# Kernel optimization log

Measured on AMD Instinct MI355X. Metric: run time of the kernel, lower is better.

Reference implementation:

```python
import jax, jax.numpy as jnp
import numpy as np


def butterfly_mult(twiddle, x):
    # twiddle: (S, M, n//2, 2, 2); x: (B, S, n); increasing_stride=True
    B, S, n = x.shape
    M = twiddle.shape[1]
    out = x
    for idx in range(M):  # loop over log2(n) stages (structural, not data dim)
        stride = 1 << idx
        g = n // (2 * stride)
        t = twiddle[:, idx].reshape(S, g, stride, 2, 2)   # (S, g, r, i, j)
        xr = out.reshape(B, S, g, 2, stride)              # (B, S, g, j, r)
        out = jnp.einsum('sgrij,bsgjr->bsgir', t, xr).reshape(B, S, n)
    return out


def butterfly_layer(x, twiddle, bias, out_size):
    # x: (..., n) with n a power of 2 (pre_process pad is a no-op)
    lead = x.shape[:-1]
    n = x.shape[-1]
    S = twiddle.shape[0]
    xb = x.reshape(-1, n)
    xb = jnp.broadcast_to(xb[:, None, :], (xb.shape[0], S, n))  # expand to nstacks
    out = butterfly_mult(twiddle, xb)
    out = out.reshape(out.shape[0], S * n)[:, :out_size] + bias[:out_size]
    return out.reshape(*lead, out_size)


def setup_inputs() -> dict:
    key = jax.random.key(0)
    ks = jax.random.split(key, 5)
    B, T, D, H = 4, 4096, 1024, 4096
    inv_sqrt2 = 1.0 / np.sqrt(2.0).astype(np.float32)
    x = jax.random.normal(ks[0], (B, T, D), jnp.float32)
    tw1 = jax.random.normal(ks[1], (4, 10, 512, 2, 2), jnp.float32) * inv_sqrt2
    b1 = jax.random.normal(ks[2], (H,), jnp.float32) * 0.02
    tw2 = jax.random.normal(ks[3], (1, 11, 1024, 2, 2), jnp.float32) * inv_sqrt2
    b2 = jax.random.normal(ks[4], (D,), jnp.float32) * 0.02
    return {"x": x, "tw1": tw1, "b1": b1, "tw2": tw2, "b2": b2}


def reference(x, tw1, b1, tw2, b2):
    # GLU: fc1 (butterfly) -> chunk -> x * sigmoid(gates) -> fc2 (butterfly)
    h = butterfly_layer(x, tw1, b1, 4096)      # (B, T, 4096)
    a, gates = jnp.split(h, 2, axis=-1)        # (B, T, 2048) each
    h = a * jax.nn.sigmoid(gates)
    return butterfly_layer(h, tw2, b2, 1024)   # (B, T, 1024)
```

## Files before the change

kernel.cpp:

```cpp
#include <hip/hip_runtime.h>
#include <cstdint>


typedef float          v4f __attribute__((ext_vector_type(4)));
typedef unsigned int   u4i __attribute__((ext_vector_type(4)));
typedef unsigned int   u2i __attribute__((ext_vector_type(2)));
typedef short          bf8 __attribute__((ext_vector_type(8)));

#define MFMA16(A, B, C) __builtin_amdgcn_mfma_f32_16x16x32_bf16(A, B, C, 0, 0, 0)

__device__ __forceinline__ unsigned pk2(float a, float b) {
    unsigned ua = __float_as_uint(a) + 0x8000u;
    unsigned ub = __float_as_uint(b) + 0x8000u;
    return __builtin_amdgcn_perm(ub, ua, 0x07060302u);
}

__device__ __forceinline__ float sigmf(float g) {
    return __builtin_amdgcn_rcpf(1.0f + __expf(-g));
}
__device__ __forceinline__ v4f sig4(v4f g) {
    v4f r; r.x = sigmf(g.x); r.y = sigmf(g.y); r.z = sigmf(g.z); r.w = sigmf(g.w);
    return r;
}

__device__ __forceinline__ int ab(int row, int hw) {
    return (row << 11) + (((hw) << 1) ^ ((row & 7) << 4));
}

__global__ void build_mats(const float* __restrict__ tw1,
                           const float* __restrict__ tw2,
                           unsigned short* __restrict__ wsm)
{
    const int mid = blockIdx.x * 2 + (threadIdx.x >> 5);
    const int c   = threadIdx.x & 31;

    const float* twf; int np, rbase, rstep, j0, scaleb = -1, l2s = 0;
    if (mid < 128)      { twf = tw1 + (mid >> 5) * 20480;        np = 512;  rbase = (mid & 31) * 32; rstep = 1;  j0 = 0; }
    else if (mid < 256) { twf = tw1 + ((mid - 128) >> 5) * 20480; np = 512; rbase = mid & 31;        rstep = 32; j0 = 5; }
    else if (mid < 320) { twf = tw2; np = 1024; rbase = (mid - 256) * 32; rstep = 1; j0 = 0; }
    else                { twf = tw2; np = 1024; l2s = mid & 31; scaleb = (mid - 320) >> 5;
                          rbase = l2s + (scaleb << 10); rstep = 32; j0 = 5; }

    float v[32];
    #pragma unroll
    for (int r = 0; r < 32; ++r) v[r] = (r == c) ? 1.0f : 0.0f;

    #pragma unroll
    for (int jj = 0; jj < 5; ++jj) {
        const int j = j0 + jj;
        #pragma unroll
        for (int pr = 0; pr < 16; ++pr) {
            const int r0   = ((pr >> jj) << (jj + 1)) | (pr & ((1 << jj) - 1));
            const int r1   = r0 | (1 << jj);
            const int p0   = rbase + r0 * rstep;
            const int tidx = ((p0 >> (j + 1)) << j) | (p0 & ((1 << j) - 1));
            const v4f T    = *(const v4f*)(twf + (size_t)(j * np + tidx) * 4);
            const float a = v[r0], b = v[r1];
            v[r0] = T.x * a + T.y * b;
            v[r1] = T.z * a + T.w * b;
        }
    }
    if (scaleb >= 0) {
        #pragma unroll
        for (int r = 0; r < 32; ++r)
            v[r] *= tw2[(size_t)(10 * 1024 + l2s + 32 * r) * 4 + scaleb];
    }
    #pragma unroll
    for (int r = 0; r < 32; ++r) {
        const int mt   = r >> 4;
        const int lane = (r & 15) + ((c >> 3) << 4);
        wsm[((size_t)(mid * 2 + mt) * 64 + lane) * 8 + (c & 7)] =
            (unsigned short)((__float_as_uint(v[r]) + 0x8000u) >> 16);
    }
}

__global__ __launch_bounds__(512) void glu_bfly(
    const float* __restrict__ x, const float* __restrict__ b1,
    const float* __restrict__ b2, const bf8* __restrict__ mats,
    float* __restrict__ out)
{
    extern __shared__ char lds[];
    char*  actA = lds;
    char*  actB = lds + 65536;
    float* b1t  = (float*)(lds + 131072);

    const int t = threadIdx.x, w = t >> 6, l = t & 63, lr = l & 15, lk = l >> 4;
    const int row0 = blockIdx.x * 32;
    const v4f vz = {0.f, 0.f, 0.f, 0.f};

    {
        const v4f* bp = (const v4f*)(b1 + t * 8);
        const v4f a = bp[0], b = bp[1];
        const float vals[8] = {a.x, a.y, a.z, a.w, b.x, b.y, b.z, b.w};
        #pragma unroll
        for (int k = 0; k < 8; ++k) {
            const int gid = t * 8 + k, s = gid >> 10, r = gid & 1023;
            b1t[(s << 10) + ((r & 31) << 5) + (r >> 5)] = vals[k];
        }
    }

    bf8 xf[4][2];
    #pragma unroll
    for (int gi = 0; gi < 4; ++gi)
    #pragma unroll
    for (int nh = 0; nh < 2; ++nh) {
        const float* xp = x + (size_t)(row0 + nh * 16 + lr) * 1024 + (w * 4 + gi) * 32 + lk * 8;
        const v4f a = *(const v4f*)xp;
        const v4f b = *(const v4f*)(xp + 4);
        u4i uu; uu.x = pk2(a.x, a.y); uu.y = pk2(a.z, a.w);
        uu.z = pk2(b.x, b.y); uu.w = pk2(b.z, b.w);
        xf[gi][nh] = __builtin_bit_cast(bf8, uu);
    }
    __syncthreads();

    unsigned z0p[4][2][2][2];
    v4f fin[4][2][2];

    #pragma unroll
    for (int h = 0; h < 2; ++h) {
        const int sa = h, sg = h + 2;

        #pragma unroll
        for (int pass = 0; pass < 2; ++pass) {
            const int s = (pass == 0) ? sa : sg;
            char* dst = (pass == 0) ? actA : actB;
            v4f acc[4][2][2];
            #pragma unroll
            for (int gi = 0; gi < 4; ++gi) {
                const int mid = s * 32 + w * 4 + gi;
                const bf8 a0 = mats[(mid * 2 + 0) * 64 + l];
                const bf8 a1 = mats[(mid * 2 + 1) * 64 + l];
                #pragma unroll
                for (int nh = 0; nh < 2; ++nh) {
                    acc[gi][nh][0] = MFMA16(a0, xf[gi][nh], vz);
                    acc[gi][nh][1] = MFMA16(a1, xf[gi][nh], vz);
                }
            }
            #pragma unroll
            for (int nh = 0; nh < 2; ++nh)
            #pragma unroll
            for (int mt = 0; mt < 2; ++mt)
            #pragma unroll
            for (int rg = 0; rg < 4; ++rg) {
                const int m = mt * 16 + lk * 4 + rg;
                u2i pv;
                pv.x = pk2(acc[0][nh][mt][rg], acc[1][nh][mt][rg]);
                pv.y = pk2(acc[2][nh][mt][rg], acc[3][nh][mt][rg]);
                *(u2i*)(dst + ab(nh * 16 + lr, 32 * m + 4 * w)) = pv;
            }
            __syncthreads();
        }

        {
            v4f uacc[4][2][2];
            #pragma unroll
            for (int li = 0; li < 4; ++li) {
                const int lg = w * 4 + li;
                v4f ha[2][2], hg[2][2];
                {
                    const int mid = 128 + sa * 32 + lg;
                    const bf8 a0 = mats[(mid * 2 + 0) * 64 + l];
                    const bf8 a1 = mats[(mid * 2 + 1) * 64 + l];
                    const bf8 f0 = *(const bf8*)(actA + ab(lr,      32 * lg + 8 * lk));
                    const bf8 f1 = *(const bf8*)(actA + ab(16 + lr, 32 * lg + 8 * lk));
                    ha[0][0] = MFMA16(a0, f0, vz); ha[0][1] = MFMA16(a1, f0, vz);
                    ha[1][0] = MFMA16(a0, f1, vz); ha[1][1] = MFMA16(a1, f1, vz);
                }
                {
                    const int mid = 128 + sg * 32 + lg;
                    const bf8 a0 = mats[(mid * 2 + 0) * 64 + l];
                    const bf8 a1 = mats[(mid * 2 + 1) * 64 + l];
                    const bf8 f0 = *(const bf8*)(actB + ab(lr,      32 * lg + 8 * lk));
                    const bf8 f1 = *(const bf8*)(actB + ab(16 + lr, 32 * lg + 8 * lk));
                    hg[0][0] = MFMA16(a0, f0, vz); hg[0][1] = MFMA16(a1, f0, vz);
                    hg[1][0] = MFMA16(a0, f1, vz); hg[1][1] = MFMA16(a1, f1, vz);
                }
                #pragma unroll
                for (int mt = 0; mt < 2; ++mt) {
                    const v4f ba = *(const v4f*)&b1t[((sa * 32 + lg) << 5) + mt * 16 + lk * 4];
                    const v4f bg = *(const v4f*)&b1t[((sg * 32 + lg) << 5) + mt * 16 + lk * 4];
                    #pragma unroll
                    for (int nh = 0; nh < 2; ++nh)
                        uacc[li][nh][mt] = (ha[nh][mt] + ba) * sig4(hg[nh][mt] + bg);
                }
            }
            __syncthreads();
            #pragma unroll
            for (int nh = 0; nh < 2; ++nh)
            #pragma unroll
            for (int mt = 0; mt < 2; ++mt)
            #pragma unroll
            for (int rg = 0; rg < 4; ++rg) {
                const int m = mt * 16 + lk * 4 + rg;
                u2i pv;
                pv.x = pk2(uacc[0][nh][mt][rg], uacc[1][nh][mt][rg]);
                pv.y = pk2(uacc[2][nh][mt][rg], uacc[3][nh][mt][rg]);
                *(u2i*)(actA + ab(nh * 16 + lr, 32 * m + 4 * w)) = pv;
            }
            __syncthreads();
        }

        {
            v4f acc[4][2][2];
            #pragma unroll
            for (int gi = 0; gi < 4; ++gi) {
                const int g = w * 4 + gi, mid = 256 + 32 * h + g;
                const bf8 a0 = mats[(mid * 2 + 0) * 64 + l];
                const bf8 a1 = mats[(mid * 2 + 1) * 64 + l];
                #pragma unroll
                for (int nh = 0; nh < 2; ++nh) {
                    const bf8 f = *(const bf8*)(actA + ab(nh * 16 + lr, 32 * g + 8 * lk));
                    acc[gi][nh][0] = MFMA16(a0, f, vz);
                    acc[gi][nh][1] = MFMA16(a1, f, vz);
                }
            }
            #pragma unroll
            for (int nh = 0; nh < 2; ++nh)
            #pragma unroll
            for (int mt = 0; mt < 2; ++mt)
            #pragma unroll
            for (int rg = 0; rg < 4; ++rg) {
                const int m = mt * 16 + lk * 4 + rg;
                u2i pv;
                pv.x = pk2(acc[0][nh][mt][rg], acc[1][nh][mt][rg]);
                pv.y = pk2(acc[2][nh][mt][rg], acc[3][nh][mt][rg]);
                *(u2i*)(actB + ab(nh * 16 + lr, 32 * m + 4 * w)) = pv;
            }
            __syncthreads();
        }

        #pragma unroll
        for (int li = 0; li < 4; ++li) {
            const int lg = w * 4 + li, mid = 320 + 32 * h + lg;
            const bf8 a0 = mats[(mid * 2 + 0) * 64 + l];
            const bf8 a1 = mats[(mid * 2 + 1) * 64 + l];
            const bf8 f0 = *(const bf8*)(actB + ab(lr,      32 * lg + 8 * lk));
            const bf8 f1 = *(const bf8*)(actB + ab(16 + lr, 32 * lg + 8 * lk));
            v4f zz[2][2];
            zz[0][0] = MFMA16(a0, f0, vz); zz[0][1] = MFMA16(a1, f0, vz);
            zz[1][0] = MFMA16(a0, f1, vz); zz[1][1] = MFMA16(a1, f1, vz);
            if (h == 0) {
                #pragma unroll
                for (int nh = 0; nh < 2; ++nh)
                #pragma unroll
                for (int mt = 0; mt < 2; ++mt) {
                    z0p[li][nh][mt][0] = pk2(zz[nh][mt].x, zz[nh][mt].y);
                    z0p[li][nh][mt][1] = pk2(zz[nh][mt].z, zz[nh][mt].w);
                }
            } else {
                #pragma unroll
                for (int nh = 0; nh < 2; ++nh)
                #pragma unroll
                for (int mt = 0; mt < 2; ++mt) {
                    v4f uz;
                    uz.x = __uint_as_float(z0p[li][nh][mt][0] << 16);
                    uz.y = __uint_as_float(z0p[li][nh][mt][0] & 0xffff0000u);
                    uz.z = __uint_as_float(z0p[li][nh][mt][1] << 16);
                    uz.w = __uint_as_float(z0p[li][nh][mt][1] & 0xffff0000u);
                    fin[li][nh][mt] = zz[nh][mt] + uz;
                }
            }
        }
    }

    #pragma unroll
    for (int nh = 0; nh < 2; ++nh) {
        #pragma unroll
        for (int mt = 0; mt < 2; ++mt)
        #pragma unroll
        for (int rg = 0; rg < 4; ++rg) {
            const int p0 = 4 * w + 32 * (mt * 16 + lk * 4 + rg);
            v4f vv;
            vv.x = fin[0][nh][mt][rg]; vv.y = fin[1][nh][mt][rg];
            vv.z = fin[2][nh][mt][rg]; vv.w = fin[3][nh][mt][rg];
            *(v4f*)(actA + (lr << 12) + ((p0 << 2) ^ ((lr & 7) << 4))) = vv;
        }
        __syncthreads();
        {
            const int row = t >> 5, c0 = (t & 31) * 4;
            #pragma unroll
            for (int i = 0; i < 8; ++i) {
                const int col = c0 + 128 * i;
                v4f ov = *(const v4f*)(actA + (row << 12) + ((col << 2) ^ ((row & 7) << 4)));
                ov += *(const v4f*)(b2 + col);
                *(v4f*)(out + (size_t)(row0 + nh * 16 + row) * 1024 + col) = ov;
            }
        }
        __syncthreads();
    }
}

extern "C" void kernel_launch(void* const* d_in, const int* in_sizes, int n_in,
                              void* d_out, int out_size, void* d_ws, size_t ws_size,
                              hipStream_t stream) {
    const float* x   = (const float*)d_in[0];
    const float* tw1 = (const float*)d_in[1];
    const float* b1  = (const float*)d_in[2];
    const float* tw2 = (const float*)d_in[3];
    const float* b2  = (const float*)d_in[4];

    build_mats<<<192, 64, 0, stream>>>(tw1, tw2, (unsigned short*)d_ws);

    (void)hipFuncSetAttribute((const void*)glu_bfly,
                              hipFuncAttributeMaxDynamicSharedMemorySize, 147456);
    glu_bfly<<<512, 512, 147456, stream>>>(x, b1, b2, (const bf8*)d_ws,
                                           (float*)d_out);
}
```

Measured before the change: 172.3 us.

## Halve rows per block, shrink LDS with bf16 bias, stage twiddles in LDS

The main kernel now handles 16 rows per block instead of 32. It launches 1024 blocks, roughly halves LDS use by storing the bias table as bf16, and adds launch_bounds(512,4) and s_setprio around MFMA bursts, all meant to raise occupancy and latency hiding. build_mats first loads each matrix's twiddles and scales into shared memory, so the dependent serial global loads inside the unrolled butterfly loop go away. In exchange, each block reuses every weight-matrix fragment over fewer rows, which doubles total weight-fragment traffic, and b1 loses precision through bf16 rounding.

```diff
diff --git a/kernel.cpp b/kernel.cpp
--- a/kernel.cpp
+++ b/kernel.cpp
@@ -15,6 +15,13 @@
     return __builtin_amdgcn_perm(ub, ua, 0x07060302u);
 }
 
+__device__ __forceinline__ v4f ub4(u2i u) {
+    v4f r;
+    r.x = __uint_as_float(u.x << 16); r.y = __uint_as_float(u.x & 0xffff0000u);
+    r.z = __uint_as_float(u.y << 16); r.w = __uint_as_float(u.y & 0xffff0000u);
+    return r;
+}
+
 __device__ __forceinline__ float sigmf(float g) {
     return __builtin_amdgcn_rcpf(1.0f + __expf(-g));
 }
@@ -23,47 +30,73 @@
     return r;
 }
 
-__device__ __forceinline__ int ab(int row, int hw) {
+__device__ __forceinline__ int ab16(int row, int hw) {
     return (row << 11) + (((hw) << 1) ^ ((row & 7) << 4));
+}
+
+struct MP { const float* twf; int np, rbase, rstep, j0; };
+__device__ __forceinline__ MP mparams(int mid, const float* tw1, const float* tw2) {
+    MP p;
+    if (mid < 128)      { p.twf = tw1 + (mid >> 5) * 20480;         p.np = 512;  p.rbase = (mid & 31) * 32; p.rstep = 1;  p.j0 = 0; }
+    else if (mid < 256) { p.twf = tw1 + ((mid - 128) >> 5) * 20480; p.np = 512;  p.rbase = mid & 31;        p.rstep = 32; p.j0 = 5; }
+    else if (mid < 320) { p.twf = tw2; p.np = 1024; p.rbase = (mid - 256) * 32; p.rstep = 1;  p.j0 = 0; }
+    else                { p.twf = tw2; p.np = 1024;
+                          p.rbase = (mid & 31) + (((mid - 320) >> 5) << 10);    p.rstep = 32; p.j0 = 5; }
+    return p;
 }
 
 __global__ void build_mats(const float* __restrict__ tw1,
                            const float* __restrict__ tw2,
                            unsigned short* __restrict__ wsm)
 {
-    const int mid = blockIdx.x * 2 + (threadIdx.x >> 5);
-    const int c   = threadIdx.x & 31;
-
-    const float* twf; int np, rbase, rstep, j0, scaleb = -1, l2s = 0;
-    if (mid < 128)      { twf = tw1 + (mid >> 5) * 20480;        np = 512;  rbase = (mid & 31) * 32; rstep = 1;  j0 = 0; }
-    else if (mid < 256) { twf = tw1 + ((mid - 128) >> 5) * 20480; np = 512; rbase = mid & 31;        rstep = 32; j0 = 5; }
-    else if (mid < 320) { twf = tw2; np = 1024; rbase = (mid - 256) * 32; rstep = 1; j0 = 0; }
-    else                { twf = tw2; np = 1024; l2s = mid & 31; scaleb = (mid - 320) >> 5;
-                          rbase = l2s + (scaleb << 10); rstep = 32; j0 = 5; }
-
+    __shared__ v4f   tlds[160];
+    __shared__ float slds[64];
+    const int t = threadIdx.x;
+    const int midb = blockIdx.x * 2;
+
+    #pragma unroll
+    for (int qq = 0; qq < 3; ++qq) {
+        const int q = t + qq * 64;
+        if (q < 160) {
+            const int ml = (q >= 80) ? 1 : 0, rem = q - ml * 80;
+            const int jj = rem >> 4, pr = rem & 15;
+            const MP p = mparams(midb + ml, tw1, tw2);
+            const int j  = p.j0 + jj;
+            const int r0 = ((pr >> jj) << (jj + 1)) | (pr & ((1 << jj) - 1));
+            const int pp = p.rbase + r0 * p.rstep;
+            const int tidx = ((pp >> (j + 1)) << j) | (pp & ((1 << j) - 1));
+            tlds[q] = *(const v4f*)(p.twf + (size_t)(j * p.np + tidx) * 4);
+        }
+    }
+    {
+        const int ml = t >> 5, r = t & 31, mid = midb + ml;
+        if (mid >= 320) {
+            const int l2s = mid & 31, sb = (mid - 320) >> 5;
+            slds[t] = tw2[(size_t)(10 * 1024 + l2s + 32 * r) * 4 + sb];
+        }
+    }
+    __syncthreads();
+
+    const int ml = t >> 5, c = t & 31, mid = midb + ml;
     float v[32];
     #pragma unroll
     for (int r = 0; r < 32; ++r) v[r] = (r == c) ? 1.0f : 0.0f;
 
     #pragma unroll
     for (int jj = 0; jj < 5; ++jj) {
-        const int j = j0 + jj;
         #pragma unroll
         for (int pr = 0; pr < 16; ++pr) {
-            const int r0   = ((pr >> jj) << (jj + 1)) | (pr & ((1 << jj) - 1));
-            const int r1   = r0 | (1 << jj);
-            const int p0   = rbase + r0 * rstep;
-            const int tidx = ((p0 >> (j + 1)) << j) | (p0 & ((1 << j) - 1));
-            const v4f T    = *(const v4f*)(twf + (size_t)(j * np + tidx) * 4);
+            const int r0 = ((pr >> jj) << (jj + 1)) | (pr & ((1 << jj) - 1));
+            const int r1 = r0 | (1 << jj);
+            const v4f T  = tlds[ml * 80 + jj * 16 + pr];
             const float a = v[r0], b = v[r1];
             v[r0] = T.x * a + T.y * b;
             v[r1] = T.z * a + T.w * b;
         }
     }
-    if (scaleb >= 0) {
-        #pragma unroll
-        for (int r = 0; r < 32; ++r)
-            v[r] *= tw2[(size_t)(10 * 1024 + l2s + 32 * r) * 4 + scaleb];
+    if (mid >= 320) {
+        #pragma unroll
+        for (int r = 0; r < 32; ++r) v[r] *= slds[ml * 32 + r];
     }
     #pragma unroll
     for (int r = 0; r < 32; ++r) {
@@ -74,18 +107,18 @@
     }
 }
 
-__global__ __launch_bounds__(512) void glu_bfly(
+__global__ __launch_bounds__(512, 4) void glu_bfly(
     const float* __restrict__ x, const float* __restrict__ b1,
     const float* __restrict__ b2, const bf8* __restrict__ mats,
     float* __restrict__ out)
 {
     extern __shared__ char lds[];
-    char*  actA = lds;
-    char*  actB = lds + 65536;
-    float* b1t  = (float*)(lds + 131072);
+    char*           actA  = lds;
+    char*           actB  = lds + 32768;
+    unsigned short* b1t16 = (unsigned short*)(lds + 65536);
 
     const int t = threadIdx.x, w = t >> 6, l = t & 63, lr = l & 15, lk = l >> 4;
-    const int row0 = blockIdx.x * 32;
+    const int row0 = blockIdx.x * 16;
     const v4f vz = {0.f, 0.f, 0.f, 0.f};
 
     {
@@ -95,26 +128,23 @@
         #pragma unroll
         for (int k = 0; k < 8; ++k) {
             const int gid = t * 8 + k, s = gid >> 10, r = gid & 1023;
-            b1t[(s << 10) + ((r & 31) << 5) + (r >> 5)] = vals[k];
-        }
-    }
-
-    bf8 xf[4][2];
-    #pragma unroll
-    for (int gi = 0; gi < 4; ++gi)
-    #pragma unroll
-    for (int nh = 0; nh < 2; ++nh) {
-        const float* xp = x + (size_t)(row0 + nh * 16 + lr) * 1024 + (w * 4 + gi) * 32 + lk * 8;
-        const v4f a = *(const v4f*)xp;
-        const v4f b = *(const v4f*)(xp + 4);
+            b1t16[(s << 10) + ((r & 31) << 5) + (r >> 5)] =
+                (unsigned short)((__float_as_uint(vals[k]) + 0x8000u) >> 16);
+        }
+    }
+
+    bf8 xf[4];
+    #pragma unroll
+    for (int gi = 0; gi < 4; ++gi) {
+        const float* xp = x + (size_t)(row0 + lr) * 1024 + (w * 4 + gi) * 32 + lk * 8;
+        const v4f a = *(const v4f*)xp, b = *(const v4f*)(xp + 4);
         u4i uu; uu.x = pk2(a.x, a.y); uu.y = pk2(a.z, a.w);
         uu.z = pk2(b.x, b.y); uu.w = pk2(b.z, b.w);
-        xf[gi][nh] = __builtin_bit_cast(bf8, uu);
-    }
-    __syncthreads();
-
-    unsigned z0p[4][2][2][2];
-    v4f fin[4][2][2];
+        xf[gi] = __builtin_bit_cast(bf8, uu);
+    }
+
+    unsigned z0p[4][2][2];
+    v4f fin[4][2];
 
     #pragma unroll
     for (int h = 0; h < 2; ++h) {
@@ -122,109 +152,92 @@
 
         #pragma unroll
         for (int pass = 0; pass < 2; ++pass) {
-            const int s = (pass == 0) ? sa : sg;
-            char* dst = (pass == 0) ? actA : actB;
-            v4f acc[4][2][2];
+            const int s = pass ? sg : sa;
+            char* dst = pass ? actB : actA;
+            v4f acc[2][4];
+            __builtin_amdgcn_s_setprio(1);
+            #pragma unroll
+            for (int mt = 0; mt < 2; ++mt)
             #pragma unroll
             for (int gi = 0; gi < 4; ++gi) {
-                const int mid = s * 32 + w * 4 + gi;
-                const bf8 a0 = mats[(mid * 2 + 0) * 64 + l];
-                const bf8 a1 = mats[(mid * 2 + 1) * 64 + l];
-                #pragma unroll
-                for (int nh = 0; nh < 2; ++nh) {
-                    acc[gi][nh][0] = MFMA16(a0, xf[gi][nh], vz);
-                    acc[gi][nh][1] = MFMA16(a1, xf[gi][nh], vz);
-                }
-            }
-            #pragma unroll
-            for (int nh = 0; nh < 2; ++nh)
+                const bf8 am = mats[((s * 32 + w * 4 + gi) * 2 + mt) * 64 + l];
+                acc[mt][gi] = MFMA16(am, xf[gi], vz);
+            }
+            __builtin_amdgcn_s_setprio(0);
             #pragma unroll
             for (int mt = 0; mt < 2; ++mt)
             #pragma unroll
             for (int rg = 0; rg < 4; ++rg) {
                 const int m = mt * 16 + lk * 4 + rg;
                 u2i pv;
-                pv.x = pk2(acc[0][nh][mt][rg], acc[1][nh][mt][rg]);
-                pv.y = pk2(acc[2][nh][mt][rg], acc[3][nh][mt][rg]);
-                *(u2i*)(dst + ab(nh * 16 + lr, 32 * m + 4 * w)) = pv;
+                pv.x = pk2(acc[mt][0][rg], acc[mt][1][rg]);
+                pv.y = pk2(acc[mt][2][rg], acc[mt][3][rg]);
+                *(u2i*)(dst + ab16(lr, 32 * m + 4 * w)) = pv;
             }
             __syncthreads();
         }
 
         {
-            v4f uacc[4][2][2];
+            v4f uacc[4][2];
             #pragma unroll
             for (int li = 0; li < 4; ++li) {
                 const int lg = w * 4 + li;
-                v4f ha[2][2], hg[2][2];
-                {
-                    const int mid = 128 + sa * 32 + lg;
-                    const bf8 a0 = mats[(mid * 2 + 0) * 64 + l];
-                    const bf8 a1 = mats[(mid * 2 + 1) * 64 + l];
-                    const bf8 f0 = *(const bf8*)(actA + ab(lr,      32 * lg + 8 * lk));
-                    const bf8 f1 = *(const bf8*)(actA + ab(16 + lr, 32 * lg + 8 * lk));
-                    ha[0][0] = MFMA16(a0, f0, vz); ha[0][1] = MFMA16(a1, f0, vz);
-                    ha[1][0] = MFMA16(a0, f1, vz); ha[1][1] = MFMA16(a1, f1, vz);
-                }
-                {
-                    const int mid = 128 + sg * 32 + lg;
-                    const bf8 a0 = mats[(mid * 2 + 0) * 64 + l];
-                    const bf8 a1 = mats[(mid * 2 + 1) * 64 + l];
-                    const bf8 f0 = *(const bf8*)(actB + ab(lr,      32 * lg + 8 * lk));
-                    const bf8 f1 = *(const bf8*)(actB + ab(16 + lr, 32 * lg + 8 * lk));
-                    hg[0][0] = MFMA16(a0, f0, vz); hg[0][1] = MFMA16(a1, f0, vz);
-                    hg[1][0] = MFMA16(a0, f1, vz); hg[1][1] = MFMA16(a1, f1, vz);
-                }
-                #pragma unroll
-                for (int mt = 0; mt < 2; ++mt) {
-                    const v4f ba = *(const v4f*)&b1t[((sa * 32 + lg) << 5) + mt * 16 + lk * 4];
-                    const v4f bg = *(const v4f*)&b1t[((sg * 32 + lg) << 5) + mt * 16 + lk * 4];
-                    #pragma unroll
-                    for (int nh = 0; nh < 2; ++nh)
-                        uacc[li][nh][mt] = (ha[nh][mt] + ba) * sig4(hg[nh][mt] + bg);
-                }
+                const bf8 fa = *(const bf8*)(actA + ab16(lr, 32 * lg + 8 * lk));
+                const bf8 fg = *(const bf8*)(actB + ab16(lr, 32 * lg + 8 * lk));
+                const int mida = 128 + sa * 32 + lg, midg = 128 + sg * 32 + lg;
+                const bf8 aa0 = mats[(mida * 2 + 0) * 64 + l];
+                const bf8 aa1 = mats[(mida * 2 + 1) * 64 + l];
+                const bf8 ag0 = mats[(midg * 2 + 0) * 64 + l];
+                const bf8 ag1 = mats[(midg * 2 + 1) * 64 + l];
+                __builtin_amdgcn_s_setprio(1);
+                const v4f ha0 = MFMA16(aa0, fa, vz), ha1 = MFMA16(aa1, fa, vz);
+                const v4f hg0 = MFMA16(ag0, fg, vz), hg1 = MFMA16(ag1, fg, vz);
+                __builtin_amdgcn_s_setprio(0);
+                const int bia = ((sa * 32 + lg) << 5) + lk * 4;
+                const int big = ((sg * 32 + lg) << 5) + lk * 4;
+                const v4f ba0 = ub4(*(const u2i*)&b1t16[bia]);
+                const v4f ba1 = ub4(*(const u2i*)&b1t16[bia + 16]);
+                const v4f bg0 = ub4(*(const u2i*)&b1t16[big]);
+                const v4f bg1 = ub4(*(const u2i*)&b1t16[big + 16]);
+                uacc[li][0] = (ha0 + ba0) * sig4(hg0 + bg0);
+                uacc[li][1] = (ha1 + ba1) * sig4(hg1 + bg1);
             }
             __syncthreads();
-            #pragma unroll
-            for (int nh = 0; nh < 2; ++nh)
             #pragma unroll
             for (int mt = 0; mt < 2; ++mt)
             #pragma unroll
             for (int rg = 0; rg < 4; ++rg) {
                 const int m = mt * 16 + lk * 4 + rg;
                 u2i pv;
-                pv.x = pk2(uacc[0][nh][mt][rg], uacc[1][nh][mt][rg]);
-                pv.y = pk2(uacc[2][nh][mt][rg], uacc[3][nh][mt][rg]);
-                *(u2i*)(actA + ab(nh * 16 + lr, 32 * m + 4 * w)) = pv;
+                pv.x = pk2(uacc[0][mt][rg], uacc[1][mt][rg]);
+                pv.y = pk2(uacc[2][mt][rg], uacc[3][mt][rg]);
+                *(u2i*)(actA + ab16(lr, 32 * m + 4 * w)) = pv;
             }
             __syncthreads();
         }
 
         {
-            v4f acc[4][2][2];
+            v4f acc[2][4];
             #pragma unroll
             for (int gi = 0; gi < 4; ++gi) {
                 const int g = w * 4 + gi, mid = 256 + 32 * h + g;
+                const bf8 f  = *(const bf8*)(actA + ab16(lr, 32 * g + 8 * lk));
                 const bf8 a0 = mats[(mid * 2 + 0) * 64 + l];
                 const bf8 a1 = mats[(mid * 2 + 1) * 64 + l];
-                #pragma unroll
-                for (int nh = 0; nh < 2; ++nh) {
-                    const bf8 f = *(const bf8*)(actA + ab(nh * 16 + lr, 32 * g + 8 * lk));
-                    acc[gi][nh][0] = MFMA16(a0, f, vz);
-                    acc[gi][nh][1] = MFMA16(a1, f, vz);
-                }
-            }
-            #pragma unroll
-            for (int nh = 0; nh < 2; ++nh)
+                __builtin_amdgcn_s_setprio(1);
+                acc[0][gi] = MFMA16(a0, f, vz);
+                acc[1][gi] = MFMA16(a1, f, vz);
+                __builtin_amdgcn_s_setprio(0);
+            }
             #pragma unroll
             for (int mt = 0; mt < 2; ++mt)
             #pragma unroll
             for (int rg = 0; rg < 4; ++rg) {
                 const int m = mt * 16 + lk * 4 + rg;
                 u2i pv;
-                pv.x = pk2(acc[0][nh][mt][rg], acc[1][nh][mt][rg]);
-                pv.y = pk2(acc[2][nh][mt][rg], acc[3][nh][mt][rg]);
-                *(u2i*)(actB + ab(nh * 16 + lr, 32 * m + 4 * w)) = pv;
+                pv.x = pk2(acc[mt][0][rg], acc[mt][1][rg]);
+                pv.y = pk2(acc[mt][2][rg], acc[mt][3][rg]);
+                *(u2i*)(actB + ab16(lr, 32 * m + 4 * w)) = pv;
             }
             __syncthreads();
         }
@@ -232,61 +245,46 @@
         #pragma unroll
         for (int li = 0; li < 4; ++li) {
             const int lg = w * 4 + li, mid = 320 + 32 * h + lg;
+            const bf8 f  = *(const bf8*)(actB + ab16(lr, 32 * lg + 8 * lk));
             const bf8 a0 = mats[(mid * 2 + 0) * 64 + l];
             const bf8 a1 = mats[(mid * 2 + 1) * 64 + l];
-            const bf8 f0 = *(const bf8*)(actB + ab(lr,      32 * lg + 8 * lk));
-            const bf8 f1 = *(const bf8*)(actB + ab(16 + lr, 32 * lg + 8 * lk));
-            v4f zz[2][2];
-            zz[0][0] = MFMA16(a0, f0, vz); zz[0][1] = MFMA16(a1, f0, vz);
-            zz[1][0] = MFMA16(a0, f1, vz); zz[1][1] = MFMA16(a1, f1, vz);
+            __builtin_amdgcn_s_setprio(1);
+            const v4f z0 = MFMA16(a0, f, vz);
+            const v4f z1 = MFMA16(a1, f, vz);
+            __builtin_amdgcn_s_setprio(0);
             if (h == 0) {
-                #pragma unroll
-                for (int nh = 0; nh < 2; ++nh)
-                #pragma unroll
-                for (int mt = 0; mt < 2; ++mt) {
-                    z0p[li][nh][mt][0] = pk2(zz[nh][mt].x, zz[nh][mt].y);
-                    z0p[li][nh][mt][1] = pk2(zz[nh][mt].z, zz[nh][mt].w);
-                }
+                z0p[li][0][0] = pk2(z0.x, z0.y); z0p[li][0][1] = pk2(z0.z, z0.w);
+                z0p[li][1][0] = pk2(z1.x, z1.y); z0p[li][1][1] = pk2(z1.z, z1.w);
             } else {
-                #pragma unroll
-                for (int nh = 0; nh < 2; ++nh)
-                #pragma unroll
-                for (int mt = 0; mt < 2; ++mt) {
-                    v4f uz;
-                    uz.x = __uint_as_float(z0p[li][nh][mt][0] << 16);
-                    uz.y = __uint_as_float(z0p[li][nh][mt][0] & 0xffff0000u);
-                    uz.z = __uint_as_float(z0p[li][nh][mt][1] << 16);
-                    uz.w = __uint_as_float(z0p[li][nh][mt][1] & 0xffff0000u);
-                    fin[li][nh][mt] = zz[nh][mt] + uz;
-                }
-            }
-        }
-    }
-
-    #pragma unroll
-    for (int nh = 0; nh < 2; ++nh) {
-        #pragma unroll
-        for (int mt = 0; mt < 2; ++mt)
-        #pragma unroll
-        for (int rg = 0; rg < 4; ++rg) {
-            const int p0 = 4 * w + 32 * (mt * 16 + lk * 4 + rg);
-            v4f vv;
-            vv.x = fin[0][nh][mt][rg]; vv.y = fin[1][nh][mt][rg];
-            vv.z = fin[2][nh][mt][rg]; vv.w = fin[3][nh][mt][rg];
-            *(v4f*)(actA + (lr << 12) + ((p0 << 2) ^ ((lr & 7) << 4))) = vv;
-        }
-        __syncthreads();
-        {
-            const int row = t >> 5, c0 = (t & 31) * 4;
-            #pragma unroll
-            for (int i = 0; i < 8; ++i) {
-                const int col = c0 + 128 * i;
-                v4f ov = *(const v4f*)(actA + (row << 12) + ((col << 2) ^ ((row & 7) << 4)));
-                ov += *(const v4f*)(b2 + col);
-                *(v4f*)(out + (size_t)(row0 + nh * 16 + row) * 1024 + col) = ov;
-            }
-        }
-        __syncthreads();
+                u2i u0; u0.x = z0p[li][0][0]; u0.y = z0p[li][0][1];
+                u2i u1; u1.x = z0p[li][1][0]; u1.y = z0p[li][1][1];
+                fin[li][0] = z0 + ub4(u0);
+                fin[li][1] = z1 + ub4(u1);
+            }
+        }
+    }
+
+    __syncthreads();
+    #pragma unroll
+    for (int mt = 0; mt < 2; ++mt)
+    #pragma unroll
+    for (int rg = 0; rg < 4; ++rg) {
+        const int p0 = 4 * w + 32 * (mt * 16 + lk * 4 + rg);
+        v4f vv;
+        vv.x = fin[0][mt][rg]; vv.y = fin[1][mt][rg];
+        vv.z = fin[2][mt][rg]; vv.w = fin[3][mt][rg];
+        *(v4f*)(lds + (lr << 12) + ((p0 << 2) ^ ((lr & 7) << 4))) = vv;
+    }
+    __syncthreads();
+    {
+        const int row = t >> 5, c0 = (t & 31) * 4;
+        #pragma unroll
+        for (int i = 0; i < 8; ++i) {
+            const int col = c0 + 128 * i;
+            v4f ov = *(const v4f*)(lds + (row << 12) + ((col << 2) ^ ((row & 7) << 4)));
+            ov += *(const v4f*)(b2 + col);
+            *(v4f*)(out + (size_t)(row0 + row) * 1024 + col) = ov;
+        }
     }
 }
 
@@ -302,7 +300,7 @@
     build_mats<<<192, 64, 0, stream>>>(tw1, tw2, (unsigned short*)d_ws);
 
     (void)hipFuncSetAttribute((const void*)glu_bfly,
-                              hipFuncAttributeMaxDynamicSharedMemorySize, 147456);
-    glu_bfly<<<512, 512, 147456, stream>>>(x, b1, b2, (const bf8*)d_ws,
+                              hipFuncAttributeMaxDynamicSharedMemorySize, 73728);
+    glu_bfly<<<1024, 512, 73728, stream>>>(x, b1, b2, (const bf8*)d_ws,
                                            (float*)d_out);
 }
```

Result: faster. 158.6 us (-8.0%).
